# Optimization experiments

Hardware: AMD Instinct MI355X
Metric: run time of the kernel (lower is better)

The kernel has to match this reference:

```python
import jax, jax.numpy as jnp
import numpy as np

N = 50000
E = 800000
IN_C, HID_C, OUT_C = 128, 256, 128
BN_EPS = 1e-5


def setup_inputs() -> dict:
    key = jax.random.key(0)
    ks = jax.random.split(key, 10)
    inp = {
        "x": jax.random.normal(ks[0], (N, IN_C), dtype=jnp.float32),
        "edge_index": jax.random.randint(ks[1], (2, E), 0, N, dtype=jnp.int64),
        # Layer 1 SAGEConv (PyG semantics): out = lin_l(mean_agg) + lin_r(x)
        "W1l": jax.random.normal(ks[2], (IN_C, HID_C), dtype=jnp.float32) * (1.0 / np.sqrt(IN_C)),
        "b1l": jnp.zeros((HID_C,), dtype=jnp.float32),
        "W1r": jax.random.normal(ks[3], (IN_C, HID_C), dtype=jnp.float32) * (1.0 / np.sqrt(IN_C)),
        # BatchNorm1d params for layer 1
        "gamma1": jnp.ones((HID_C,), dtype=jnp.float32),
        "beta1": jnp.zeros((HID_C,), dtype=jnp.float32),
        # Layer 2 SAGEConv
        "W2l": jax.random.normal(ks[4], (HID_C, OUT_C), dtype=jnp.float32) * (1.0 / np.sqrt(HID_C)),
        "b2l": jnp.zeros((OUT_C,), dtype=jnp.float32),
        "W2r": jax.random.normal(ks[5], (HID_C, OUT_C), dtype=jnp.float32) * (1.0 / np.sqrt(HID_C)),
    }
    return inp


def _mean_aggregate(x, src, dst):
    # mean of source-node features over each destination node; empty nbhd -> 0
    summed = jax.ops.segment_sum(x[src], dst, num_segments=N)           # [N, d]
    cnt = jax.ops.segment_sum(jnp.ones((src.shape[0],), x.dtype), dst, num_segments=N)
    return summed / jnp.maximum(cnt, 1.0)[:, None]


def _batchnorm_train(h, gamma, beta):
    mu = jnp.mean(h, axis=0)
    var = jnp.mean(jnp.square(h - mu), axis=0)  # biased variance (BN train mode)
    return (h - mu) * jax.lax.rsqrt(var + BN_EPS) * gamma + beta


def reference(x, edge_index, W1l, b1l, W1r, gamma1, beta1, W2l, b2l, W2r):
    src, dst = edge_index[0], edge_index[1]
    # Layer 1: SAGEConv -> BN -> ReLU (dropout p=0)
    agg1 = _mean_aggregate(x, src, dst)
    h = agg1 @ W1l + b1l + x @ W1r
    h = _batchnorm_train(h, gamma1, beta1)
    h = jax.nn.relu(h)
    # Layer 2: SAGEConv only (no BN: len(bns)==1; no activation: last layer)
    agg2 = _mean_aggregate(h, src, dst)
    out = agg2 @ W2l + b2l + h @ W2r
    return out
```

## Files before the change

### kernel.cpp

```cpp
#include <hip/hip_runtime.h>

#define NN 50000
#define NPAD 50176
#define MPAD 50048
#define NE 800000
#define BN_EPS 1e-5f

#define NSEG 782
#define NBKT 49

typedef __attribute__((ext_vector_type(8))) short bf16x8;
typedef __attribute__((ext_vector_type(4))) float f32x4;

__device__ __forceinline__ void atomAddF(float* p, float v) { unsafeAtomicAdd(p, v); }

__device__ __forceinline__ float bf2f(ushort u) {
    union { uint i; float f; } v; v.i = ((uint)u) << 16; return v.f;
}
__device__ __forceinline__ ushort f2bf(float f) {
    union { uint i; float f; } v; v.f = f;
    uint u = v.i;
    return (ushort)((u + 0x7FFFu + ((u >> 16) & 1u)) >> 16);
}

__global__ __launch_bounds__(256) void k_zero(int4* __restrict__ dst) {
    if (threadIdx.x < 128) dst[threadIdx.x] = make_int4(0, 0, 0, 0);
}

__global__ __launch_bounds__(256) void k_part(const int* __restrict__ ei,
                                              int2* __restrict__ seg,
                                              int* __restrict__ cnt2,
                                              int* __restrict__ boff2) {
    __shared__ int lcnt[NBKT];
    __shared__ int lboff[NBKT];
    __shared__ int2 lbuf[1024];
    const int b = blockIdx.x, t = threadIdx.x;
    if (t < NBKT) lcnt[t] = 0;
    __syncthreads();
    int src[4], dst[4], rk[4], bkt[4];
    const int e0 = b * 1024;
    #pragma unroll
    for (int j = 0; j < 4; ++j) {
        int e = e0 + t + j * 256;
        if (e < NE) {
            src[j] = ei[e];
            dst[j] = ei[NE + e];
            bkt[j] = dst[j] >> 10;
            rk[j] = atomicAdd(&lcnt[bkt[j]], 1);
        } else rk[j] = -1;
    }
    __syncthreads();
    if (t < 64) {
        int v = (t < NBKT) ? lcnt[t] : 0;
        int x = v;
        #pragma unroll
        for (int off = 1; off < 64; off <<= 1) {
            int y = __shfl_up(x, off);
            if (t >= off) x += y;
        }
        if (t < NBKT) lboff[t] = x - v;
    }
    __syncthreads();
    #pragma unroll
    for (int j = 0; j < 4; ++j)
        if (rk[j] >= 0) lbuf[lboff[bkt[j]] + rk[j]] = make_int2(src[j], dst[j]);
    __syncthreads();
    const int total = lboff[NBKT - 1] + lcnt[NBKT - 1];
    for (int i = t; i < total; i += 256) seg[e0 + i] = lbuf[i];
    if (t < NBKT) { cnt2[b * NBKT + t] = lcnt[t]; boff2[b * NBKT + t] = lboff[t]; }
}

__global__ __launch_bounds__(1024) void k_cnt(const int2* __restrict__ seg,
                                              const int* __restrict__ cnt2,
                                              const int* __restrict__ boff2,
                                              int* __restrict__ cnt) {
    __shared__ int lrk[1024];
    const int k = blockIdx.x, t = threadIdx.x;
    lrk[t] = 0;
    __syncthreads();
    const int node0 = k << 10;
    const int g = t >> 3, l = t & 7;
    for (int b = g; b < NSEG; b += 128) {
        const int n = cnt2[b * NBKT + k];
        const int base = b * 1024 + boff2[b * NBKT + k];
        for (int i = l; i < n; i += 8)
            atomicAdd(&lrk[seg[base + i].y - node0], 1);
    }
    __syncthreads();
    cnt[node0 + t] = lrk[t];
}

__global__ __launch_bounds__(1024) void k_rank(const int2* __restrict__ seg,
                                               const int* __restrict__ cnt2,
                                               const int* __restrict__ boff2,
                                               const int* __restrict__ rowptr,
                                               int* __restrict__ csr_src) {
    __shared__ int lrk[1024];
    const int k = blockIdx.x, t = threadIdx.x;
    lrk[t] = 0;
    __syncthreads();
    const int node0 = k << 10;
    const int g = t >> 3, l = t & 7;
    for (int b = g; b < NSEG; b += 128) {
        const int n = cnt2[b * NBKT + k];
        const int base = b * 1024 + boff2[b * NBKT + k];
        for (int i = l; i < n; i += 8) {
            int2 e = seg[base + i];
            int rank = atomicAdd(&lrk[e.y - node0], 1);
            csr_src[rowptr[e.y] + rank] = e.x;
        }
    }
}

__global__ __launch_bounds__(256) void k_scanA(const int* __restrict__ cnt,
                                               int* __restrict__ locpre, int* __restrict__ bsum) {
    const int b = blockIdx.x, t = threadIdx.x;
    const int base = b * 1024 + t * 4;
    int4 v = *reinterpret_cast<const int4*>(&cnt[base]);
    int s = v.x + v.y + v.z + v.w;
    __shared__ int sm[256];
    sm[t] = s;
    __syncthreads();
    for (int off = 1; off < 256; off <<= 1) {
        int y = (t >= off) ? sm[t - off] : 0;
        __syncthreads();
        sm[t] += y;
        __syncthreads();
    }
    int excl = sm[t] - s;
    locpre[base + 0] = excl;
    locpre[base + 1] = excl + v.x;
    locpre[base + 2] = excl + v.x + v.y;
    locpre[base + 3] = excl + v.x + v.y + v.z;
    if (t == 255) bsum[b] = sm[255];
}

__global__ __launch_bounds__(256) void k_scanC(const int* __restrict__ cnt,
                                               const int* __restrict__ locpre,
                                               const int* __restrict__ bsum,
                                               int* __restrict__ rowptr,
                                               float* __restrict__ invc) {
    __shared__ int sm[64];
    const int b = blockIdx.x, t = threadIdx.x;
    const int nb = NPAD / 1024;
    if (t < nb) sm[t] = bsum[t];
    __syncthreads();
    int off = 0;
    for (int j = 0; j < b; ++j) off += sm[j];
    const int base = b * 1024 + t * 4;
    #pragma unroll
    for (int k = 0; k < 4; ++k) {
        int i = base + k;
        if (i < NN) {
            rowptr[i] = locpre[i] + off;
            invc[i] = 1.0f / fmaxf((float)cnt[i], 1.0f);
        }
    }
    if (b == 0 && t == 0) rowptr[NN] = NE;
}

__global__ __launch_bounds__(256) void k_prep(const float* __restrict__ x, ushort* __restrict__ xb,
                                              const float* __restrict__ W1l, const float* __restrict__ W1r,
                                              const float* __restrict__ W2l, const float* __restrict__ W2r,
                                              ushort* __restrict__ Wt1, ushort* __restrict__ Wt2) {
    if (blockIdx.x < 3125) {
        unsigned g = blockIdx.x * 256u + threadIdx.x;
        const float4* p = reinterpret_cast<const float4*>(x) + (size_t)g * 2;
        float4 a = p[0], b = p[1];
        uint4 w;
        w.x = (uint)f2bf(a.x) | ((uint)f2bf(a.y) << 16);
        w.y = (uint)f2bf(a.z) | ((uint)f2bf(a.w) << 16);
        w.z = (uint)f2bf(b.x) | ((uint)f2bf(b.y) << 16);
        w.w = (uint)f2bf(b.z) | ((uint)f2bf(b.w) << 16);
        *reinterpret_cast<uint4*>(&xb[(size_t)g * 8]) = w;
    } else {
        int g = (blockIdx.x - 3125) * 256 + threadIdx.x;
        if (g < 65536) {
            int n = g >> 8, k = g & 255;
            float v = (k < 128) ? W1l[k * 256 + n] : W1r[(k - 128) * 256 + n];
            Wt1[n * 256 + k] = f2bf(v);
        } else {
            int g2 = g - 65536;
            int n = g2 >> 8, k = g2 & 255;
            float v = (n < 128) ? W2l[k * 128 + n] : W2r[k * 128 + (n - 128)];
            Wt2[n * 256 + k] = f2bf(v);
        }
    }
}

template <bool FINAL>
__global__ __launch_bounds__(256) void k_agg128(const ushort* __restrict__ feat,
                                                const int* __restrict__ rowptr,
                                                const int* __restrict__ csr_src,
                                                const float* __restrict__ invc,
                                                const float* __restrict__ z,
                                                const float* __restrict__ bias,
                                                ushort* __restrict__ aggb,
                                                float* __restrict__ outf) {
    int gw = (blockIdx.x * 256 + threadIdx.x) >> 6;
    int lane = threadIdx.x & 63;
    if (gw >= NN) return;
    const int grp = lane >> 4, sl = lane & 15;
    const int beg = rowptr[gw], end = rowptr[gw + 1];
    float acc[8] = {};
    int e = beg + grp;
    for (; e + 12 < end; e += 16) {
        int s0 = csr_src[e];
        int s1 = csr_src[e + 4];
        int s2 = csr_src[e + 8];
        int s3 = csr_src[e + 12];
        uint4 u0 = *reinterpret_cast<const uint4*>(&feat[(size_t)s0 * 128 + sl * 8]);
        uint4 u1 = *reinterpret_cast<const uint4*>(&feat[(size_t)s1 * 128 + sl * 8]);
        uint4 u2 = *reinterpret_cast<const uint4*>(&feat[(size_t)s2 * 128 + sl * 8]);
        uint4 u3 = *reinterpret_cast<const uint4*>(&feat[(size_t)s3 * 128 + sl * 8]);
        acc[0] += bf2f((ushort)u0.x) + bf2f((ushort)u1.x) + bf2f((ushort)u2.x) + bf2f((ushort)u3.x);
        acc[1] += bf2f((ushort)(u0.x >> 16)) + bf2f((ushort)(u1.x >> 16)) + bf2f((ushort)(u2.x >> 16)) + bf2f((ushort)(u3.x >> 16));
        acc[2] += bf2f((ushort)u0.y) + bf2f((ushort)u1.y) + bf2f((ushort)u2.y) + bf2f((ushort)u3.y);
        acc[3] += bf2f((ushort)(u0.y >> 16)) + bf2f((ushort)(u1.y >> 16)) + bf2f((ushort)(u2.y >> 16)) + bf2f((ushort)(u3.y >> 16));
        acc[4] += bf2f((ushort)u0.z) + bf2f((ushort)u1.z) + bf2f((ushort)u2.z) + bf2f((ushort)u3.z);
        acc[5] += bf2f((ushort)(u0.z >> 16)) + bf2f((ushort)(u1.z >> 16)) + bf2f((ushort)(u2.z >> 16)) + bf2f((ushort)(u3.z >> 16));
        acc[6] += bf2f((ushort)u0.w) + bf2f((ushort)u1.w) + bf2f((ushort)u2.w) + bf2f((ushort)u3.w);
        acc[7] += bf2f((ushort)(u0.w >> 16)) + bf2f((ushort)(u1.w >> 16)) + bf2f((ushort)(u2.w >> 16)) + bf2f((ushort)(u3.w >> 16));
    }
    for (; e < end; e += 4) {
        int s0 = csr_src[e];
        uint4 u0 = *reinterpret_cast<const uint4*>(&feat[(size_t)s0 * 128 + sl * 8]);
        acc[0] += bf2f((ushort)u0.x); acc[1] += bf2f((ushort)(u0.x >> 16));
        acc[2] += bf2f((ushort)u0.y); acc[3] += bf2f((ushort)(u0.y >> 16));
        acc[4] += bf2f((ushort)u0.z); acc[5] += bf2f((ushort)(u0.z >> 16));
        acc[6] += bf2f((ushort)u0.w); acc[7] += bf2f((ushort)(u0.w >> 16));
    }
    #pragma unroll
    for (int i = 0; i < 8; ++i) {
        acc[i] += __shfl_xor(acc[i], 16);
        acc[i] += __shfl_xor(acc[i], 32);
    }
    if (grp == 0) {
        const float ic = invc[gw];
        if constexpr (FINAL) {
            const float* zp = &z[(size_t)gw * 128 + sl * 8];
            float4 z0 = *reinterpret_cast<const float4*>(zp);
            float4 z1 = *reinterpret_cast<const float4*>(zp + 4);
            float4 b0 = *reinterpret_cast<const float4*>(&bias[sl * 8]);
            float4 b1 = *reinterpret_cast<const float4*>(&bias[sl * 8 + 4]);
            float4 o0, o1;
            o0.x = fmaf(acc[0], ic, z0.x + b0.x);
            o0.y = fmaf(acc[1], ic, z0.y + b0.y);
            o0.z = fmaf(acc[2], ic, z0.z + b0.z);
            o0.w = fmaf(acc[3], ic, z0.w + b0.w);
            o1.x = fmaf(acc[4], ic, z1.x + b1.x);
            o1.y = fmaf(acc[5], ic, z1.y + b1.y);
            o1.z = fmaf(acc[6], ic, z1.z + b1.z);
            o1.w = fmaf(acc[7], ic, z1.w + b1.w);
            float* op = &outf[(size_t)gw * 128 + sl * 8];
            *reinterpret_cast<float4*>(op) = o0;
            *reinterpret_cast<float4*>(op + 4) = o1;
        } else {
            uint4 o;
            o.x = (uint)f2bf(acc[0] * ic) | ((uint)f2bf(acc[1] * ic) << 16);
            o.y = (uint)f2bf(acc[2] * ic) | ((uint)f2bf(acc[3] * ic) << 16);
            o.z = (uint)f2bf(acc[4] * ic) | ((uint)f2bf(acc[5] * ic) << 16);
            o.w = (uint)f2bf(acc[6] * ic) | ((uint)f2bf(acc[7] * ic) << 16);
            *reinterpret_cast<uint4*>(&aggb[(size_t)gw * 128 + sl * 8]) = o;
        }
    }
}

template <int K1, int K2, int NC, bool STATS, bool BN1, int OUTMODE>
__global__ __launch_bounds__(256, 4) void k_mm(const ushort* __restrict__ A1,
                                               const ushort* __restrict__ A2,
                                               const ushort* __restrict__ Wt,
                                               const float* __restrict__ bias,
                                               const float* __restrict__ sc,
                                               const float* __restrict__ sh,
                                               float* __restrict__ bnsums,
                                               ushort* __restrict__ outb,
                                               float* __restrict__ outf) {
    constexpr int KT = K1 + K2;
    constexpr int NIT = KT / 32;
    constexpr int BSTR = 264;
    constexpr int NWG = 1564, Q = NWG / 8, R = NWG % 8;
    __shared__ ushort Bs[64 * BSTR];
    __shared__ float sred[4][4][16][2];
    const int t = threadIdx.x;
    const int lane = t & 63, wid = t >> 6;
    const int bid = blockIdx.x;
    const int xcd = bid & 7, idx = bid >> 3;
    const int logical = (xcd < R ? xcd * (Q + 1) : R * (Q + 1) + (xcd - R) * Q) + idx;
    const int r0 = (logical >> 2) * 128, c0 = (logical & 3) * 64;
    const int lr = lane & 15, lg = lane >> 4;
    const int wrow = r0 + wid * 32;

    #pragma unroll
    for (int i = 0; i < 64 * KT / 8 / 256; ++i) {
        int idx2 = i * 256 + t;
        int col = idx2 / (KT / 8);
        int slot = idx2 % (KT / 8);
        *reinterpret_cast<bf16x8*>(&Bs[col * BSTR + slot * 8]) =
            *reinterpret_cast<const bf16x8*>(&Wt[(size_t)(c0 + col) * KT + slot * 8]);
    }
    __syncthreads();

    f32x4 acc[2][4] = {};
    #pragma unroll
    for (int it = 0; it < NIT; ++it) {
        const int kt = it * 32;
        const ushort* __restrict__ Ap = (kt < K1) ? A1 : A2;
        const int AK = (kt < K1) ? K1 : K2;
        const int ak = (kt < K1) ? kt : kt - K1;
        bf16x8 af[2];
        #pragma unroll
        for (int mi = 0; mi < 2; ++mi) {
            af[mi] = *reinterpret_cast<const bf16x8*>(
                &Ap[(size_t)(wrow + mi * 16 + lr) * AK + ak + lg * 8]);
            if constexpr (BN1) {
                const int cb = kt + lg * 8;
                float4 s0 = *reinterpret_cast<const float4*>(&sc[cb]);
                float4 s1 = *reinterpret_cast<const float4*>(&sc[cb + 4]);
                float4 h0 = *reinterpret_cast<const float4*>(&sh[cb]);
                float4 h1 = *reinterpret_cast<const float4*>(&sh[cb + 4]);
                float fsv[8] = {s0.x, s0.y, s0.z, s0.w, s1.x, s1.y, s1.z, s1.w};
                float fhv[8] = {h0.x, h0.y, h0.z, h0.w, h1.x, h1.y, h1.z, h1.w};
                #pragma unroll
                for (int j = 0; j < 8; ++j) {
                    float f = bf2f((ushort)af[mi][j]);
                    f = fmaxf(fmaf(f, fsv[j], fhv[j]), 0.f);
                    af[mi][j] = (short)f2bf(f);
                }
            }
        }
        bf16x8 bf[4];
        #pragma unroll
        for (int nj = 0; nj < 4; ++nj)
            bf[nj] = *reinterpret_cast<bf16x8*>(&Bs[(nj * 16 + lr) * BSTR + kt + lg * 8]);
        #pragma unroll
        for (int mi = 0; mi < 2; ++mi)
            #pragma unroll
            for (int nj = 0; nj < 4; ++nj)
                acc[mi][nj] = __builtin_amdgcn_mfma_f32_16x16x32_bf16(af[mi], bf[nj], acc[mi][nj], 0, 0, 0);
    }

    float ssum[4] = {}, s2sum[4] = {};
    #pragma unroll
    for (int nj = 0; nj < 4; ++nj) {
        const int col = c0 + nj * 16 + lr;
        float bv = 0.f;
        if constexpr (OUTMODE == 0) bv = bias[col];
        #pragma unroll
        for (int mi = 0; mi < 2; ++mi) {
            const int rbase = wrow + mi * 16;
            if (rbase + 16 > NN) continue;
            #pragma unroll
            for (int reg = 0; reg < 4; ++reg) {
                const int row = rbase + lg * 4 + reg;
                float d = acc[mi][nj][reg] + bv;
                if constexpr (STATS) { ssum[nj] += d; s2sum[nj] += d * d; }
                if constexpr (OUTMODE == 0) {
                    outb[(size_t)row * NC + col] = f2bf(d);
                } else {
                    if (col < 128) outb[(size_t)row * 128 + col] = f2bf(d);
                    else outf[(size_t)row * 128 + (col - 128)] = d;
                }
            }
        }
    }
    if constexpr (STATS) {
        #pragma unroll
        for (int nj = 0; nj < 4; ++nj) {
            ssum[nj] += __shfl_xor(ssum[nj], 16); ssum[nj] += __shfl_xor(ssum[nj], 32);
            s2sum[nj] += __shfl_xor(s2sum[nj], 16); s2sum[nj] += __shfl_xor(s2sum[nj], 32);
        }
        if (lane < 16) {
            #pragma unroll
            for (int nj = 0; nj < 4; ++nj) {
                sred[wid][nj][lane][0] = ssum[nj];
                sred[wid][nj][lane][1] = s2sum[nj];
            }
        }
        __syncthreads();
        if (wid == 0 && lane < 16) {
            #pragma unroll
            for (int nj = 0; nj < 4; ++nj) {
                const int col = c0 + nj * 16 + lane;
                float s = sred[0][nj][lane][0] + sred[1][nj][lane][0] + sred[2][nj][lane][0] + sred[3][nj][lane][0];
                float s2 = sred[0][nj][lane][1] + sred[1][nj][lane][1] + sred[2][nj][lane][1] + sred[3][nj][lane][1];
                atomAddF(&bnsums[col], s);
                atomAddF(&bnsums[256 + col], s2);
            }
        }
    }
}

__global__ void k_bnfin(const float* __restrict__ sums, const float* __restrict__ gamma,
                        const float* __restrict__ beta, float* __restrict__ sc,
                        float* __restrict__ sh) {
    int c = threadIdx.x;
    float mu = sums[c] * (1.0f / NN);
    float var = sums[256 + c] * (1.0f / NN) - mu * mu;
    float s = gamma[c] * rsqrtf(var + BN_EPS);
    sc[c] = s;
    sh[c] = beta[c] - mu * s;
}

extern "C" void kernel_launch(void* const* d_in, const int* in_sizes, int n_in,
                              void* d_out, int out_size, void* d_ws, size_t ws_size,
                              hipStream_t stream) {
    const float* x    = (const float*)d_in[0];
    const int*   ei   = (const int*)d_in[1];
    const float* W1l  = (const float*)d_in[2];
    const float* b1l  = (const float*)d_in[3];
    const float* W1r  = (const float*)d_in[4];
    const float* gam1 = (const float*)d_in[5];
    const float* bet1 = (const float*)d_in[6];
    const float* W2l  = (const float*)d_in[7];
    const float* b2l  = (const float*)d_in[8];
    const float* W2r  = (const float*)d_in[9];
    float* out = (float*)d_out;

    char* p = (char*)d_ws;
    ushort* xb   = (ushort*)p; p += (size_t)MPAD * 128 * 2;
    ushort* hb   = (ushort*)p; p += (size_t)MPAD * 256 * 2;
    ushort* aggb = (ushort*)p; p += (size_t)MPAD * 128 * 2;
    ushort* y2b  = (ushort*)p; p += (size_t)MPAD * 128 * 2;
    float*  zf   = (float*)p;  p += (size_t)MPAD * 128 * 4;
    ushort* Wt1  = (ushort*)p; p += 256 * 256 * 2;
    ushort* Wt2  = (ushort*)p; p += 256 * 256 * 2;
    int*   cnt    = (int*)p;   p += (size_t)NPAD * 4;
    float* bnsums = (float*)p; p += 512 * 4;
    float* bnsc   = (float*)p; p += 256 * 4;
    float* bnsh   = (float*)p; p += 256 * 4;
    float* invc   = (float*)p; p += (size_t)NPAD * 4;
    int*   rowptr = (int*)p;   p += (size_t)(NPAD + 4) * 4;
    int*   csr_src= (int*)p;   p += (size_t)NE * 4;
    int2*  seg    = (int2*)p;  p += (size_t)NE * 8;
    int*   cnt2   = (int*)p;   p += (size_t)NSEG * NBKT * 4;
    int*   boff2  = (int*)p;   p += (size_t)NSEG * NBKT * 4;
    int*   locpre = (int*)aggb;
    int*   bsum   = cnt2 + NSEG * NBKT - 64;
    bsum = (int*)p; p += 64 * 4;

    k_zero<<<1, 256, 0, stream>>>((int4*)bnsums);

    k_part<<<NSEG, 256, 0, stream>>>(ei, seg, cnt2, boff2);
    k_cnt<<<NBKT, 1024, 0, stream>>>(seg, cnt2, boff2, cnt);
    k_scanA<<<NPAD / 1024, 256, 0, stream>>>(cnt, locpre, bsum);
    k_scanC<<<NPAD / 1024, 256, 0, stream>>>(cnt, locpre, bsum, rowptr, invc);
    k_rank<<<NBKT, 1024, 0, stream>>>(seg, cnt2, boff2, rowptr, csr_src);

    k_prep<<<3637, 256, 0, stream>>>(x, xb, W1l, W1r, W2l, W2r, Wt1, Wt2);

    k_agg128<false><<<12500, 256, 0, stream>>>(xb, rowptr, csr_src, invc, nullptr, nullptr, aggb, nullptr);
    k_mm<128, 128, 256, true, false, 0><<<1564, 256, 0, stream>>>(
        aggb, xb, Wt1, b1l, nullptr, nullptr, bnsums, hb, nullptr);
    k_bnfin<<<1, 256, 0, stream>>>(bnsums, gam1, bet1, bnsc, bnsh);

    k_mm<256, 0, 256, false, true, 1><<<1564, 256, 0, stream>>>(
        hb, nullptr, Wt2, nullptr, bnsc, bnsh, nullptr, y2b, zf);
    k_agg128<true><<<12500, 256, 0, stream>>>(y2b, rowptr, csr_src, invc, zf, b2l, nullptr, out);
}
```

Before: 184.6 us.

## Fuse preprocessing kernels and fold BN finalize into GEMM to cut launches

Merges zeroing, edge partitioning and bf16 conversion into one launch, fuses per-node counting with the in-bucket prefix scan, and fuses the cross-bucket offset, rowptr/invc and CSR fill into one kernel. BN scale/shift is now computed per block in the second GEMM from the raw sums, so the separate finalize launch goes away. This removes about five kernel launches and their serialization gaps. In exchange, every GEMM block redundantly recomputes the BN constants and reads them from shared memory in the inner loop, and the 1024-wide scan in shared memory adds barrier-heavy steps.

```diff
diff --git a/kernel.cpp b/kernel.cpp
--- a/kernel.cpp
+++ b/kernel.cpp
@@ -23,58 +23,90 @@
     return (ushort)((u + 0x7FFFu + ((u >> 16) & 1u)) >> 16);
 }
 
-__global__ __launch_bounds__(256) void k_zero(int4* __restrict__ dst) {
-    if (threadIdx.x < 128) dst[threadIdx.x] = make_int4(0, 0, 0, 0);
-}
-
-__global__ __launch_bounds__(256) void k_part(const int* __restrict__ ei,
-                                              int2* __restrict__ seg,
-                                              int* __restrict__ cnt2,
-                                              int* __restrict__ boff2) {
-    __shared__ int lcnt[NBKT];
-    __shared__ int lboff[NBKT];
-    __shared__ int2 lbuf[1024];
-    const int b = blockIdx.x, t = threadIdx.x;
-    if (t < NBKT) lcnt[t] = 0;
-    __syncthreads();
-    int src[4], dst[4], rk[4], bkt[4];
-    const int e0 = b * 1024;
-    #pragma unroll
-    for (int j = 0; j < 4; ++j) {
-        int e = e0 + t + j * 256;
-        if (e < NE) {
-            src[j] = ei[e];
-            dst[j] = ei[NE + e];
-            bkt[j] = dst[j] >> 10;
-            rk[j] = atomicAdd(&lcnt[bkt[j]], 1);
-        } else rk[j] = -1;
-    }
-    __syncthreads();
-    if (t < 64) {
-        int v = (t < NBKT) ? lcnt[t] : 0;
-        int x = v;
-        #pragma unroll
-        for (int off = 1; off < 64; off <<= 1) {
-            int y = __shfl_up(x, off);
-            if (t >= off) x += y;
-        }
-        if (t < NBKT) lboff[t] = x - v;
-    }
-    __syncthreads();
-    #pragma unroll
-    for (int j = 0; j < 4; ++j)
-        if (rk[j] >= 0) lbuf[lboff[bkt[j]] + rk[j]] = make_int2(src[j], dst[j]);
-    __syncthreads();
-    const int total = lboff[NBKT - 1] + lcnt[NBKT - 1];
-    for (int i = t; i < total; i += 256) seg[e0 + i] = lbuf[i];
-    if (t < NBKT) { cnt2[b * NBKT + t] = lcnt[t]; boff2[b * NBKT + t] = lboff[t]; }
-}
-
-__global__ __launch_bounds__(1024) void k_cnt(const int2* __restrict__ seg,
-                                              const int* __restrict__ cnt2,
-                                              const int* __restrict__ boff2,
-                                              int* __restrict__ cnt) {
+__global__ __launch_bounds__(256) void k_pp(const int* __restrict__ ei,
+                                            int2* __restrict__ seg,
+                                            int* __restrict__ cnt2,
+                                            int* __restrict__ boff2,
+                                            const float* __restrict__ x, ushort* __restrict__ xb,
+                                            const float* __restrict__ W1l, const float* __restrict__ W1r,
+                                            const float* __restrict__ W2l, const float* __restrict__ W2r,
+                                            ushort* __restrict__ Wt1, ushort* __restrict__ Wt2,
+                                            float* __restrict__ bnsums) {
+    const int t = threadIdx.x;
+    if (blockIdx.x < NSEG) {
+        __shared__ int lcnt[NBKT];
+        __shared__ int lboff[NBKT];
+        __shared__ int2 lbuf[1024];
+        const int b = blockIdx.x;
+        if (b == 0 && t < 128) reinterpret_cast<int4*>(bnsums)[t] = make_int4(0, 0, 0, 0);
+        if (t < NBKT) lcnt[t] = 0;
+        __syncthreads();
+        int src[4], dst[4], rk[4], bkt[4];
+        const int e0 = b * 1024;
+        #pragma unroll
+        for (int j = 0; j < 4; ++j) {
+            int e = e0 + t + j * 256;
+            if (e < NE) {
+                src[j] = ei[e];
+                dst[j] = ei[NE + e];
+                bkt[j] = dst[j] >> 10;
+                rk[j] = atomicAdd(&lcnt[bkt[j]], 1);
+            } else rk[j] = -1;
+        }
+        __syncthreads();
+        if (t < 64) {
+            int v = (t < NBKT) ? lcnt[t] : 0;
+            int y = v;
+            #pragma unroll
+            for (int off = 1; off < 64; off <<= 1) {
+                int z = __shfl_up(y, off);
+                if (t >= off) y += z;
+            }
+            if (t < NBKT) lboff[t] = y - v;
+        }
+        __syncthreads();
+        #pragma unroll
+        for (int j = 0; j < 4; ++j)
+            if (rk[j] >= 0) lbuf[lboff[bkt[j]] + rk[j]] = make_int2(src[j], dst[j]);
+        __syncthreads();
+        const int total = lboff[NBKT - 1] + lcnt[NBKT - 1];
+        for (int i = t; i < total; i += 256) seg[e0 + i] = lbuf[i];
+        if (t < NBKT) { cnt2[b * NBKT + t] = lcnt[t]; boff2[b * NBKT + t] = lboff[t]; }
+    } else {
+        const int pb = blockIdx.x - NSEG;
+        if (pb < 3125) {
+            unsigned g = pb * 256u + t;
+            const float4* p = reinterpret_cast<const float4*>(x) + (size_t)g * 2;
+            float4 a = p[0], b2 = p[1];
+            uint4 w;
+            w.x = (uint)f2bf(a.x) | ((uint)f2bf(a.y) << 16);
+            w.y = (uint)f2bf(a.z) | ((uint)f2bf(a.w) << 16);
+            w.z = (uint)f2bf(b2.x) | ((uint)f2bf(b2.y) << 16);
+            w.w = (uint)f2bf(b2.z) | ((uint)f2bf(b2.w) << 16);
+            *reinterpret_cast<uint4*>(&xb[(size_t)g * 8]) = w;
+        } else {
+            int g = (pb - 3125) * 256 + t;
+            if (g < 65536) {
+                int n = g >> 8, k = g & 255;
+                float v = (k < 128) ? W1l[k * 256 + n] : W1r[(k - 128) * 256 + n];
+                Wt1[n * 256 + k] = f2bf(v);
+            } else {
+                int g2 = g - 65536;
+                int n = g2 >> 8, k = g2 & 255;
+                float v = (n < 128) ? W2l[k * 128 + n] : W2r[k * 128 + (n - 128)];
+                Wt2[n * 256 + k] = f2bf(v);
+            }
+        }
+    }
+}
+
+__global__ __launch_bounds__(1024) void k_cntA(const int2* __restrict__ seg,
+                                               const int* __restrict__ cnt2,
+                                               const int* __restrict__ boff2,
+                                               int* __restrict__ locpre,
+                                               int* __restrict__ bsum) {
     __shared__ int lrk[1024];
+    __shared__ int sm[1024];
     const int k = blockIdx.x, t = threadIdx.x;
     lrk[t] = 0;
     __syncthreads();
@@ -87,103 +119,61 @@
             atomicAdd(&lrk[seg[base + i].y - node0], 1);
     }
     __syncthreads();
-    cnt[node0 + t] = lrk[t];
-}
-
-__global__ __launch_bounds__(1024) void k_rank(const int2* __restrict__ seg,
-                                               const int* __restrict__ cnt2,
-                                               const int* __restrict__ boff2,
-                                               const int* __restrict__ rowptr,
-                                               int* __restrict__ csr_src) {
+    int v = lrk[t];
+    sm[t] = v;
+    __syncthreads();
+    for (int off = 1; off < 1024; off <<= 1) {
+        int y = (t >= off) ? sm[t - off] : 0;
+        __syncthreads();
+        sm[t] += y;
+        __syncthreads();
+    }
+    locpre[node0 + t] = sm[t] - v;
+    if (t == 1023) bsum[k] = sm[1023];
+}
+
+__global__ __launch_bounds__(1024) void k_rankC(const int2* __restrict__ seg,
+                                                const int* __restrict__ cnt2,
+                                                const int* __restrict__ boff2,
+                                                const int* __restrict__ locpre,
+                                                const int* __restrict__ bsum,
+                                                int* __restrict__ rowptr,
+                                                float* __restrict__ invc,
+                                                int* __restrict__ csr_src) {
+    __shared__ int lbase[1024];
     __shared__ int lrk[1024];
+    __shared__ int soff_sh, stot_sh;
     const int k = blockIdx.x, t = threadIdx.x;
+    if (t < 64) {
+        int v = (t < k) ? bsum[t] : 0;
+        #pragma unroll
+        for (int off = 1; off < 64; off <<= 1) v += __shfl_xor(v, off);
+        if (t == 0) { soff_sh = v; stot_sh = bsum[k]; }
+    }
     lrk[t] = 0;
     __syncthreads();
+    const int soff = soff_sh, stot = stot_sh;
     const int node0 = k << 10;
+    const int base = locpre[node0 + t] + soff;
+    lbase[t] = base;
+    __syncthreads();
+    const int node = node0 + t;
+    if (node <= NN) {
+        if (node < NN || node == NN) rowptr[node] = base;
+        if (node < NN) {
+            int nextb = (t < 1023) ? lbase[t + 1] : soff + stot;
+            invc[node] = 1.0f / fmaxf((float)(nextb - base), 1.0f);
+        }
+    }
     const int g = t >> 3, l = t & 7;
     for (int b = g; b < NSEG; b += 128) {
         const int n = cnt2[b * NBKT + k];
-        const int base = b * 1024 + boff2[b * NBKT + k];
+        const int sb = b * 1024 + boff2[b * NBKT + k];
         for (int i = l; i < n; i += 8) {
-            int2 e = seg[base + i];
-            int rank = atomicAdd(&lrk[e.y - node0], 1);
-            csr_src[rowptr[e.y] + rank] = e.x;
-        }
-    }
-}
-
-__global__ __launch_bounds__(256) void k_scanA(const int* __restrict__ cnt,
-                                               int* __restrict__ locpre, int* __restrict__ bsum) {
-    const int b = blockIdx.x, t = threadIdx.x;
-    const int base = b * 1024 + t * 4;
-    int4 v = *reinterpret_cast<const int4*>(&cnt[base]);
-    int s = v.x + v.y + v.z + v.w;
-    __shared__ int sm[256];
-    sm[t] = s;
-    __syncthreads();
-    for (int off = 1; off < 256; off <<= 1) {
-        int y = (t >= off) ? sm[t - off] : 0;
-        __syncthreads();
-        sm[t] += y;
-        __syncthreads();
-    }
-    int excl = sm[t] - s;
-    locpre[base + 0] = excl;
-    locpre[base + 1] = excl + v.x;
-    locpre[base + 2] = excl + v.x + v.y;
-    locpre[base + 3] = excl + v.x + v.y + v.z;
-    if (t == 255) bsum[b] = sm[255];
-}
-
-__global__ __launch_bounds__(256) void k_scanC(const int* __restrict__ cnt,
-                                               const int* __restrict__ locpre,
-                                               const int* __restrict__ bsum,
-                                               int* __restrict__ rowptr,
-                                               float* __restrict__ invc) {
-    __shared__ int sm[64];
-    const int b = blockIdx.x, t = threadIdx.x;
-    const int nb = NPAD / 1024;
-    if (t < nb) sm[t] = bsum[t];
-    __syncthreads();
-    int off = 0;
-    for (int j = 0; j < b; ++j) off += sm[j];
-    const int base = b * 1024 + t * 4;
-    #pragma unroll
-    for (int k = 0; k < 4; ++k) {
-        int i = base + k;
-        if (i < NN) {
-            rowptr[i] = locpre[i] + off;
-            invc[i] = 1.0f / fmaxf((float)cnt[i], 1.0f);
-        }
-    }
-    if (b == 0 && t == 0) rowptr[NN] = NE;
-}
-
-__global__ __launch_bounds__(256) void k_prep(const float* __restrict__ x, ushort* __restrict__ xb,
-                                              const float* __restrict__ W1l, const float* __restrict__ W1r,
-                                              const float* __restrict__ W2l, const float* __restrict__ W2r,
-                                              ushort* __restrict__ Wt1, ushort* __restrict__ Wt2) {
-    if (blockIdx.x < 3125) {
-        unsigned g = blockIdx.x * 256u + threadIdx.x;
-        const float4* p = reinterpret_cast<const float4*>(x) + (size_t)g * 2;
-        float4 a = p[0], b = p[1];
-        uint4 w;
-        w.x = (uint)f2bf(a.x) | ((uint)f2bf(a.y) << 16);
-        w.y = (uint)f2bf(a.z) | ((uint)f2bf(a.w) << 16);
-        w.z = (uint)f2bf(b.x) | ((uint)f2bf(b.y) << 16);
-        w.w = (uint)f2bf(b.z) | ((uint)f2bf(b.w) << 16);
-        *reinterpret_cast<uint4*>(&xb[(size_t)g * 8]) = w;
-    } else {
-        int g = (blockIdx.x - 3125) * 256 + threadIdx.x;
-        if (g < 65536) {
-            int n = g >> 8, k = g & 255;
-            float v = (k < 128) ? W1l[k * 256 + n] : W1r[(k - 128) * 256 + n];
-            Wt1[n * 256 + k] = f2bf(v);
-        } else {
-            int g2 = g - 65536;
-            int n = g2 >> 8, k = g2 & 255;
-            float v = (n < 128) ? W2l[k * 128 + n] : W2r[k * 128 + (n - 128)];
-            Wt2[n * 256 + k] = f2bf(v);
+            int2 e = seg[sb + i];
+            int li = e.y - node0;
+            int rank = atomicAdd(&lrk[li], 1);
+            csr_src[lbase[li] + rank] = e.x;
         }
     }
 }
@@ -271,8 +261,8 @@
                                                const ushort* __restrict__ A2,
                                                const ushort* __restrict__ Wt,
                                                const float* __restrict__ bias,
-                                               const float* __restrict__ sc,
-                                               const float* __restrict__ sh,
+                                               const float* __restrict__ gamma,
+                                               const float* __restrict__ beta,
                                                float* __restrict__ bnsums,
                                                ushort* __restrict__ outb,
                                                float* __restrict__ outf) {
@@ -282,6 +272,7 @@
     constexpr int NWG = 1564, Q = NWG / 8, R = NWG % 8;
     __shared__ ushort Bs[64 * BSTR];
     __shared__ float sred[4][4][16][2];
+    __shared__ float scs[256], shs[256];
     const int t = threadIdx.x;
     const int lane = t & 63, wid = t >> 6;
     const int bid = blockIdx.x;
@@ -291,6 +282,13 @@
     const int lr = lane & 15, lg = lane >> 4;
     const int wrow = r0 + wid * 32;
 
+    if constexpr (BN1) {
+        float mu = bnsums[t & 255] * (1.0f / NN);
+        float var = bnsums[256 + (t & 255)] * (1.0f / NN) - mu * mu;
+        float s = gamma[t & 255] * rsqrtf(var + BN_EPS);
+        scs[t & 255] = s;
+        shs[t & 255] = beta[t & 255] - mu * s;
+    }
     #pragma unroll
     for (int i = 0; i < 64 * KT / 8 / 256; ++i) {
         int idx2 = i * 256 + t;
@@ -315,16 +313,10 @@
                 &Ap[(size_t)(wrow + mi * 16 + lr) * AK + ak + lg * 8]);
             if constexpr (BN1) {
                 const int cb = kt + lg * 8;
-                float4 s0 = *reinterpret_cast<const float4*>(&sc[cb]);
-                float4 s1 = *reinterpret_cast<const float4*>(&sc[cb + 4]);
-                float4 h0 = *reinterpret_cast<const float4*>(&sh[cb]);
-                float4 h1 = *reinterpret_cast<const float4*>(&sh[cb + 4]);
-                float fsv[8] = {s0.x, s0.y, s0.z, s0.w, s1.x, s1.y, s1.z, s1.w};
-                float fhv[8] = {h0.x, h0.y, h0.z, h0.w, h1.x, h1.y, h1.z, h1.w};
                 #pragma unroll
                 for (int j = 0; j < 8; ++j) {
                     float f = bf2f((ushort)af[mi][j]);
-                    f = fmaxf(fmaf(f, fsv[j], fhv[j]), 0.f);
+                    f = fmaxf(fmaf(f, scs[cb + j], shs[cb + j]), 0.f);
                     af[mi][j] = (short)f2bf(f);
                 }
             }
@@ -391,17 +383,6 @@
     }
 }
 
-__global__ void k_bnfin(const float* __restrict__ sums, const float* __restrict__ gamma,
-                        const float* __restrict__ beta, float* __restrict__ sc,
-                        float* __restrict__ sh) {
-    int c = threadIdx.x;
-    float mu = sums[c] * (1.0f / NN);
-    float var = sums[256 + c] * (1.0f / NN) - mu * mu;
-    float s = gamma[c] * rsqrtf(var + BN_EPS);
-    sc[c] = s;
-    sh[c] = beta[c] - mu * s;
-}
-
 extern "C" void kernel_launch(void* const* d_in, const int* in_sizes, int n_in,
                               void* d_out, int out_size, void* d_ws, size_t ws_size,
                               hipStream_t stream) {
@@ -425,36 +406,25 @@
     float*  zf   = (float*)p;  p += (size_t)MPAD * 128 * 4;
     ushort* Wt1  = (ushort*)p; p += 256 * 256 * 2;
     ushort* Wt2  = (ushort*)p; p += 256 * 256 * 2;
-    int*   cnt    = (int*)p;   p += (size_t)NPAD * 4;
-    float* bnsums = (float*)p; p += 512 * 4;
-    float* bnsc   = (float*)p; p += 256 * 4;
-    float* bnsh   = (float*)p; p += 256 * 4;
+    float* bnsums = (float*)p; p += 512 * 4 + 2048;
     float* invc   = (float*)p; p += (size_t)NPAD * 4;
     int*   rowptr = (int*)p;   p += (size_t)(NPAD + 4) * 4;
     int*   csr_src= (int*)p;   p += (size_t)NE * 4;
     int2*  seg    = (int2*)p;  p += (size_t)NE * 8;
     int*   cnt2   = (int*)p;   p += (size_t)NSEG * NBKT * 4;
     int*   boff2  = (int*)p;   p += (size_t)NSEG * NBKT * 4;
+    int*   bsum   = (int*)p;   p += 64 * 4;
     int*   locpre = (int*)aggb;
-    int*   bsum   = cnt2 + NSEG * NBKT - 64;
-    bsum = (int*)p; p += 64 * 4;
-
-    k_zero<<<1, 256, 0, stream>>>((int4*)bnsums);
-
-    k_part<<<NSEG, 256, 0, stream>>>(ei, seg, cnt2, boff2);
-    k_cnt<<<NBKT, 1024, 0, stream>>>(seg, cnt2, boff2, cnt);
-    k_scanA<<<NPAD / 1024, 256, 0, stream>>>(cnt, locpre, bsum);
-    k_scanC<<<NPAD / 1024, 256, 0, stream>>>(cnt, locpre, bsum, rowptr, invc);
-    k_rank<<<NBKT, 1024, 0, stream>>>(seg, cnt2, boff2, rowptr, csr_src);
-
-    k_prep<<<3637, 256, 0, stream>>>(x, xb, W1l, W1r, W2l, W2r, Wt1, Wt2);
+
+    k_pp<<<NSEG + 3637, 256, 0, stream>>>(ei, seg, cnt2, boff2,
+                                          x, xb, W1l, W1r, W2l, W2r, Wt1, Wt2, bnsums);
+    k_cntA<<<NBKT, 1024, 0, stream>>>(seg, cnt2, boff2, locpre, bsum);
+    k_rankC<<<NBKT, 1024, 0, stream>>>(seg, cnt2, boff2, locpre, bsum, rowptr, invc, csr_src);
 
     k_agg128<false><<<12500, 256, 0, stream>>>(xb, rowptr, csr_src, invc, nullptr, nullptr, aggb, nullptr);
     k_mm<128, 128, 256, true, false, 0><<<1564, 256, 0, stream>>>(
         aggb, xb, Wt1, b1l, nullptr, nullptr, bnsums, hb, nullptr);
-    k_bnfin<<<1, 256, 0, stream>>>(bnsums, gam1, bet1, bnsc, bnsh);
-
     k_mm<256, 0, 256, false, true, 1><<<1564, 256, 0, stream>>>(
-        hb, nullptr, Wt2, nullptr, bnsc, bnsh, nullptr, y2b, zf);
+        hb, nullptr, Wt2, nullptr, gam1, bet1, bnsums, y2b, zf);
     k_agg128<true><<<12500, 256, 0, stream>>>(y2b, rowptr, csr_src, invc, zf, b2l, nullptr, out);
 }
```

New measurement: 160.9 us. -12.8%, faster.
